# Kernel optimization log

Measured on AMD Instinct MI355X. Metric: run time of the kernel, lower is better.

## Reference

```python
import jax, jax.numpy as jnp
import numpy as np

NUM_HEADS = 4
HID = 64
NUM_LAYERS = 3
NEG_SLOPE = 0.2  # PyG GATConv default


def setup_inputs() -> dict:
    key = jax.random.key(0)
    ks = jax.random.split(key, 6)
    B, N, D = 64, 512, 64
    return {
        "embeddings": jax.random.normal(ks[0], (B, N, D), jnp.float32),
        "lin_w": jax.random.normal(ks[1], (NUM_LAYERS, NUM_HEADS * HID, D), jnp.float32) * 0.1,
        "att_src": jax.random.normal(ks[2], (NUM_LAYERS, NUM_HEADS, HID), jnp.float32) * 0.1,
        "att_dst": jax.random.normal(ks[3], (NUM_LAYERS, NUM_HEADS, HID), jnp.float32) * 0.1,
        "conv_b": jnp.zeros((NUM_LAYERS, HID), jnp.float32),
        "readout_w": jax.random.normal(ks[4], (D, HID), jnp.float32) * 0.1,
        "readout_b": jnp.zeros((D,), jnp.float32),
    }


def reference(embeddings, lin_w, att_src, att_dst, conv_b, readout_w, readout_b):
    # Graph is fully connected (combinations + reversed) and PyG GATConv adds
    # self-loops by default -> attention softmax over ALL nodes j for each i.
    B, N, _ = embeddings.shape
    x = embeddings
    for l in range(NUM_LAYERS):
        h = jnp.einsum('bnd,od->bno', x, lin_w[l]).reshape(B, N, NUM_HEADS, HID)  # [B,N,H,C]
        a_src = jnp.einsum('bnhc,hc->bnh', h, att_src[l])  # per source node j
        a_dst = jnp.einsum('bnhc,hc->bnh', h, att_dst[l])  # per target node i
        e = a_dst[:, :, None, :] + a_src[:, None, :, :]    # [B,i,j,H]
        e = jnp.where(e >= 0, e, NEG_SLOPE * e)            # LeakyReLU(0.2)
        alpha = jax.nn.softmax(e, axis=2)                  # softmax over neighbors j
        out = jnp.einsum('bijh,bjhc->bihc', alpha, h).mean(axis=2) + conv_b[l]  # concat=False -> head mean
        x = jax.nn.relu(out)
    pooled = x.mean(axis=1)                                # mean over nodes
    return pooled @ readout_w.T + readout_b                # [B, D]
```

## Files before the change

### kernel.cpp

```cpp
#include <hip/hip_runtime.h>
#include <math.h>


using short8  = __attribute__((ext_vector_type(8))) short;
using floatx4 = __attribute__((ext_vector_type(4))) float;

__device__ inline unsigned short f2bf(float f) {
    union { float f; unsigned u; } v; v.f = f;
    unsigned u = v.u + 0x7FFFu + ((v.u >> 16) & 1u);
    return (unsigned short)(u >> 16);
}
__device__ inline float bf2f(unsigned short s) {
    union { float f; unsigned u; } v; v.u = ((unsigned)s) << 16;
    return v.f;
}

__device__ inline void cvt8(const float4 a, const float4 b, short8& hi, short8& lo) {
    float f[8] = {a.x, a.y, a.z, a.w, b.x, b.y, b.z, b.w};
    short8 H, L;
#pragma unroll
    for (int i = 0; i < 8; ++i) {
        unsigned short h = f2bf(f[i]);
        H[i] = (short)h;
        L[i] = (short)f2bf(f[i] - bf2f(h));
    }
    hi = H; lo = L;
}

__global__ __launch_bounds__(256) void linprep_kernel(const float* __restrict__ x,
                                                      const float* __restrict__ W,
                                                      const float* __restrict__ att_src,
                                                      const float* __restrict__ att_dst,
                                                      float* __restrict__ hT,
                                                      int* __restrict__ g_rank,
                                                      float* __restrict__ g_E1,
                                                      float* __restrict__ g_E2,
                                                      float* __restrict__ g_aZ,
                                                      float* __restrict__ g_bZ,
                                                      int* __restrict__ g_k) {
    __shared__ unsigned short WH[64 * 72], WL[64 * 72];
    __shared__ float sA[512], dA[512];
    __shared__ int   s_idxE[512];
    __shared__ float z1suf[513], z2pre[513];
    __shared__ float wred[8];

    const int t  = threadIdx.x;
    const int bh = blockIdx.x;
    const int b  = bh >> 2;
    const int ct = bh & 3;
    const int c0 = ct * 64;

#pragma unroll
    for (int q = 0; q < 4; ++q) {
        int f = q * 256 + t;
        int wrow = f >> 4, d4 = f & 15;
        float4 v = *(const float4*)(W + (size_t)(c0 + wrow) * 64 + d4 * 4);
        unsigned short h0 = f2bf(v.x), h1 = f2bf(v.y), h2 = f2bf(v.z), h3 = f2bf(v.w);
        ushort4 hi = make_ushort4(h0, h1, h2, h3);
        ushort4 lo = make_ushort4(f2bf(v.x - bf2f(h0)), f2bf(v.y - bf2f(h1)),
                                  f2bf(v.z - bf2f(h2)), f2bf(v.w - bf2f(h3)));
        *(ushort4*)&WH[wrow * 72 + d4 * 4] = hi;
        *(ushort4*)&WL[wrow * 72 + d4 * 4] = lo;
    }
    __syncthreads();

    const int lane = t & 63, wv = t >> 6;
    const int mrow = lane & 15, quad = lane >> 4;

    short8 bhf[4][2], blf[4][2];
#pragma unroll
    for (int g = 0; g < 4; ++g)
#pragma unroll
        for (int kk = 0; kk < 2; ++kk) {
            int ko = kk * 32 + quad * 8;
            bhf[g][kk] = *(const short8*)&WH[(g * 16 + mrow) * 72 + ko];
            blf[g][kk] = *(const short8*)&WL[(g * 16 + mrow) * 72 + ko];
        }
    float as_g[4], ad_g[4];
#pragma unroll
    for (int g = 0; g < 4; ++g) {
        as_g[g] = att_src[c0 + g * 16 + mrow];
        ad_g[g] = att_dst[c0 + g * 16 + mrow];
    }

    const float* xbase = x + (size_t)(b * 512 + mrow) * 64 + quad * 8;
    float4 nxa = *(const float4*)(xbase + (size_t)wv * 1024);
    float4 nxb = *(const float4*)(xbase + (size_t)wv * 1024 + 4);
    float4 nxc = *(const float4*)(xbase + (size_t)wv * 1024 + 32);
    float4 nxd = *(const float4*)(xbase + (size_t)wv * 1024 + 36);

#pragma unroll 1
    for (int tl = wv; tl < 32; tl += 4) {
        float4 xa = nxa, xb = nxb, xc = nxc, xd = nxd;
        if (tl + 4 < 32) {
            const float* nb = xbase + (size_t)(tl + 4) * 1024;
            nxa = *(const float4*)(nb);
            nxb = *(const float4*)(nb + 4);
            nxc = *(const float4*)(nb + 32);
            nxd = *(const float4*)(nb + 36);
        }
        short8 ah0, al0, ah1, al1;
        cvt8(xa, xb, ah0, al0);
        cvt8(xc, xd, ah1, al1);

        floatx4 acc[4];
#pragma unroll
        for (int g = 0; g < 4; ++g) {
            floatx4 a = {0.f, 0.f, 0.f, 0.f};
            a = __builtin_amdgcn_mfma_f32_16x16x32_bf16(ah0, bhf[g][0], a, 0, 0, 0);
            a = __builtin_amdgcn_mfma_f32_16x16x32_bf16(ah1, bhf[g][1], a, 0, 0, 0);
            a = __builtin_amdgcn_mfma_f32_16x16x32_bf16(ah0, blf[g][0], a, 0, 0, 0);
            a = __builtin_amdgcn_mfma_f32_16x16x32_bf16(ah1, blf[g][1], a, 0, 0, 0);
            a = __builtin_amdgcn_mfma_f32_16x16x32_bf16(al0, bhf[g][0], a, 0, 0, 0);
            a = __builtin_amdgcn_mfma_f32_16x16x32_bf16(al1, bhf[g][1], a, 0, 0, 0);
            acc[g] = a;
        }

        const int r0 = b * 512 + tl * 16;
#pragma unroll
        for (int g = 0; g < 4; ++g) {
            *(float4*)&hT[(size_t)(ct * 64 + g * 16 + mrow) * 32768 + r0 + quad * 4] =
                make_float4(acc[g][0], acc[g][1], acc[g][2], acc[g][3]);
        }

        float ps[4], pd[4];
#pragma unroll
        for (int reg = 0; reg < 4; ++reg) {
            ps[reg] = acc[0][reg] * as_g[0] + acc[1][reg] * as_g[1]
                    + acc[2][reg] * as_g[2] + acc[3][reg] * as_g[3];
            pd[reg] = acc[0][reg] * ad_g[0] + acc[1][reg] * ad_g[1]
                    + acc[2][reg] * ad_g[2] + acc[3][reg] * ad_g[3];
        }
#pragma unroll
        for (int m = 1; m <= 8; m <<= 1) {
#pragma unroll
            for (int reg = 0; reg < 4; ++reg) {
                ps[reg] += __shfl_xor(ps[reg], m, 64);
                pd[reg] += __shfl_xor(pd[reg], m, 64);
            }
        }
        if (mrow < 4) {
            sA[tl * 16 + quad * 4 + mrow] = ps[mrow];
            dA[tl * 16 + quad * 4 + mrow] = pd[mrow];
        }
    }
    __syncthreads();

    const int wid = t >> 6;

    float dreg[2];
    for (int rr = 0; rr < 2; ++rr) dreg[rr] = dA[t + rr * 256];

    float v0 = sA[2 * t], v1 = sA[2 * t + 1];
    int id0 = 2 * t, id1 = 2 * t + 1;
    for (int k = 2; k <= 512; k <<= 1) {
        for (int j = k >> 1; j >= 1; j >>= 1) {
            bool asc = ((t & (k >> 1)) == 0);
            if (j == 1) {
                bool sw = asc ? (v0 > v1) : (v0 < v1);
                if (sw) { float tv = v0; v0 = v1; v1 = tv; int ti = id0; id0 = id1; id1 = ti; }
            } else if (j <= 64) {
                int m = j >> 1;
                float w0 = __shfl_xor(v0, m, 64);
                int  wi0 = __shfl_xor(id0, m, 64);
                float w1 = __shfl_xor(v1, m, 64);
                int  wi1 = __shfl_xor(id1, m, 64);
                bool low = ((t & m) == 0);
                bool wantmin = (low == asc);
                if (wantmin ? (w0 < v0) : (w0 > v0)) { v0 = w0; id0 = wi0; }
                if (wantmin ? (w1 < v1) : (w1 > v1)) { v1 = w1; id1 = wi1; }
            } else {
                int m = j >> 1;
                sA[2 * t] = v0; sA[2 * t + 1] = v1;
                s_idxE[2 * t] = id0; s_idxE[2 * t + 1] = id1;
                __syncthreads();
                int tp = t ^ m;
                float w0 = sA[2 * tp], w1 = sA[2 * tp + 1];
                int wi0 = s_idxE[2 * tp], wi1 = s_idxE[2 * tp + 1];
                bool low = ((t & m) == 0);
                bool wantmin = (low == asc);
                if (wantmin ? (w0 < v0) : (w0 > v0)) { v0 = w0; id0 = wi0; }
                if (wantmin ? (w1 < v1) : (w1 > v1)) { v1 = w1; id1 = wi1; }
                __syncthreads();
            }
        }
    }

    sA[2 * t] = v0; sA[2 * t + 1] = v1;
    __syncthreads();
    const float M = sA[511];
    float e1_0 = __expf(v0 - M), e1_1 = __expf(v1 - M);
    float e2_0 = __expf(0.2f * (v0 - M)), e2_1 = __expf(0.2f * (v1 - M));
    {
        const int base = bh * 512;
        g_E1[base + id0] = e1_0;  g_E1[base + id1] = e1_1;
        g_E2[base + id0] = e2_0;  g_E2[base + id1] = e2_1;
        g_rank[base + id0] = 2 * t;  g_rank[base + id1] = 2 * t + 1;
    }

    float S1 = e1_0 + e1_1, S2 = e2_0 + e2_1;
    float i1 = S1, i2 = S2;
    for (int off = 1; off < 64; off <<= 1) {
        float u1 = __shfl_up(i1, off, 64);
        float u2 = __shfl_up(i2, off, 64);
        if (lane >= off) { i1 += u1; i2 += u2; }
    }
    if (lane == 63) { wred[wid] = i1; wred[4 + wid] = i2; }
    __syncthreads();
    float off1 = 0.f, off2 = 0.f;
    for (int w = 0; w < wid; ++w) { off1 += wred[w]; off2 += wred[4 + w]; }
    const float T1 = wred[0] + wred[1] + wred[2] + wred[3];
    const float T2 = wred[4] + wred[5] + wred[6] + wred[7];
    float pre1 = off1 + i1 - S1;
    float pre2 = off2 + i2 - S2;
    z1suf[2 * t] = T1 - pre1;
    z1suf[2 * t + 1] = T1 - pre1 - e1_0;
    z2pre[2 * t] = pre2;
    z2pre[2 * t + 1] = pre2 + e2_0;
    if (t == 0) { z1suf[512] = 0.f; z2pre[512] = T2; }
    __syncthreads();

    for (int rr = 0; rr < 2; ++rr) {
        int i = t + rr * 256;
        float d = dreg[rr];
        int lo = 0, hi = 512;
        while (lo < hi) {
            int mid = (lo + hi) >> 1;
            if (d + sA[mid] >= 0.f) hi = mid; else lo = mid + 1;
        }
        int k = lo;
        float g = d + M;
        float G = (g >= 0.f) ? g : 0.2f * g;
        float al = __expf(g - G);
        float be = __expf(0.2f * g - G);
        float Z = al * z1suf[k] + be * z2pre[k];
        float inv = 1.0f / Z;
        g_aZ[bh * 512 + i] = al * inv;
        g_bZ[bh * 512 + i] = be * inv;
        g_k[bh * 512 + i]  = k;
    }
}

__global__ __launch_bounds__(256) void attn_agg_fin(const float* __restrict__ hT,
                                                    const int* __restrict__ g_rank,
                                                    const float* __restrict__ g_E1,
                                                    const float* __restrict__ g_E2,
                                                    const float* __restrict__ g_aZ,
                                                    const float* __restrict__ g_bZ,
                                                    const int* __restrict__ g_k,
                                                    const float* __restrict__ bias,
                                                    float* __restrict__ x) {
    const int b  = blockIdx.x & 63;
    const int cg = blockIdx.x >> 6;
    const int c0 = cg * 2;
    const int t = threadIdx.x;
    const int lane = t & 63, wv = t >> 6;

    __shared__ float A1[4][2][512], A2[4][2][512];
    __shared__ float tots[4][2];

    {
        const int bh = b * 4 + wv;
        const int base = bh * 512;
        const float* hTb = hT + (size_t)(wv * 64 + c0) * 32768 + (size_t)b * 512;
#pragma unroll
        for (int it = 0; it < 8; ++it) {
            int j = it * 64 + lane;
            int rk = g_rank[base + j];
            float e1 = g_E1[base + j];
            float e2 = g_E2[base + j];
            float h0 = hTb[j];
            float h1 = hTb[32768 + j];
            int pk = ((rk & 7) << 6) | (rk >> 3);
            A1[wv][0][pk] = e1 * h0;  A2[wv][0][pk] = e2 * h0;
            A1[wv][1][pk] = e1 * h1;  A2[wv][1][pk] = e2 * h1;
        }
#pragma unroll
        for (int cc = 0; cc < 2; ++cc) {
            float v1[8], v2[8];
#pragma unroll
            for (int i = 0; i < 8; ++i) {
                v1[i] = A1[wv][cc][i * 64 + lane];
                v2[i] = A2[wv][cc][i * 64 + lane];
            }
            float s1 = 0.f, s2 = 0.f;
#pragma unroll
            for (int i = 0; i < 8; ++i) { s1 += v1[i]; s2 += v2[i]; }
            float suf = s1;
#pragma unroll
            for (int off = 1; off < 64; off <<= 1) {
                float u = __shfl_down(suf, off, 64);
                if (lane + off < 64) suf += u;
            }
            float run = suf - s1;
            float pre = s2;
#pragma unroll
            for (int off = 1; off < 64; off <<= 1) {
                float u = __shfl_up(pre, off, 64);
                if (lane >= off) pre += u;
            }
            float run2 = pre - s2;
            if (lane == 63) tots[wv][cc] = pre;
#pragma unroll
            for (int i = 7; i >= 0; --i) { run += v1[i]; v1[i] = run; }
#pragma unroll
            for (int i = 0; i < 8; ++i) { float tv = v2[i]; v2[i] = run2; run2 += tv; }
#pragma unroll
            for (int i = 0; i < 8; ++i) {
                A1[wv][cc][i * 64 + lane] = v1[i];
                A2[wv][cc][i * 64 + lane] = v2[i];
            }
        }
    }
    __syncthreads();

    const float bv0 = bias[c0], bv1 = bias[c0 + 1];
#pragma unroll
    for (int rr = 0; rr < 2; ++rr) {
        const int i = t + rr * 256;
        float a0 = 0.f, a1 = 0.f;
#pragma unroll
        for (int head = 0; head < 4; ++head) {
            const int base = (b * 4 + head) * 512;
            float aZ = g_aZ[base + i];
            float bZ = g_bZ[base + i];
            int k = g_k[base + i];
            if (k < 512) {
                int pk = ((k & 7) << 6) | (k >> 3);
                a0 += aZ * A1[head][0][pk] + bZ * A2[head][0][pk];
                a1 += aZ * A1[head][1][pk] + bZ * A2[head][1][pk];
            } else {
                a0 += bZ * tots[head][0];
                a1 += bZ * tots[head][1];
            }
        }
        float2 o = make_float2(fmaxf(0.25f * a0 + bv0, 0.f),
                               fmaxf(0.25f * a1 + bv1, 0.f));
        *(float2*)&x[(size_t)(b * 512 + i) * 64 + c0] = o;
    }
}

__global__ __launch_bounds__(256) void readout_kernel(const float* __restrict__ x,
                                                      const float* __restrict__ rw,
                                                      const float* __restrict__ rb,
                                                      float* __restrict__ out) {
    __shared__ float red[4][64];
    __shared__ float pooled[64];
    int b = blockIdx.x, t = threadIdx.x;
    int c = t & 63, q = t >> 6;
    float acc = 0.f;
    for (int n = q; n < 512; n += 4) acc += x[((size_t)b * 512 + n) * 64 + c];
    red[q][c] = acc;
    __syncthreads();
    if (t < 64) pooled[t] = (red[0][t] + red[1][t] + red[2][t] + red[3][t]) * (1.0f / 512.0f);
    __syncthreads();
    if (t < 64) {
        float a = rb[t];
        for (int cc = 0; cc < 64; ++cc) a += pooled[cc] * rw[t * 64 + cc];
        out[b * 64 + t] = a;
    }
}

extern "C" void kernel_launch(void* const* d_in, const int* in_sizes, int n_in,
                              void* d_out, int out_size, void* d_ws, size_t ws_size,
                              hipStream_t stream) {
    const float* emb       = (const float*)d_in[0];
    const float* lin_w     = (const float*)d_in[1];
    const float* att_src   = (const float*)d_in[2];
    const float* att_dst   = (const float*)d_in[3];
    const float* conv_b    = (const float*)d_in[4];
    const float* readout_w = (const float*)d_in[5];
    const float* readout_b = (const float*)d_in[6];
    float* out = (float*)d_out;

    float* ws   = (float*)d_ws;
    float* xbuf = ws;
    float* hT   = ws + 2097152;
    float* meta = ws + 10485760;

    int*   g_rank = (int*)meta;
    float* g_E1   = meta + 131072;
    float* g_E2   = meta + 262144;
    float* g_aZ   = meta + 393216;
    float* g_bZ   = meta + 524288;
    int*   g_k    = (int*)(meta + 655360);

    for (int l = 0; l < 3; ++l) {
        const float* xin = (l == 0) ? emb : xbuf;
        linprep_kernel<<<256, 256, 0, stream>>>(xin, lin_w + (size_t)l * 16384,
                                                att_src + l * 256, att_dst + l * 256,
                                                hT, g_rank, g_E1, g_E2, g_aZ, g_bZ, g_k);
        attn_agg_fin<<<2048, 256, 0, stream>>>(hT, g_rank, g_E1, g_E2, g_aZ, g_bZ, g_k,
                                               conv_b + l * 64, xbuf);
    }
    readout_kernel<<<64, 256, 0, stream>>>(xbuf, readout_w, readout_b, out);
}
```

Measured before the change: 237.2 us.

## Fuse linear, attention prep and aggregation into one per-batch layer kernel

Merges the linear/prep kernel and the aggregation kernel into a single kernel with one 1024-thread block per batch element, each 256-thread group handling one head. The sort results, exponentials, normalizers and rank indices now stay in LDS instead of round-tripping through global memory, and one launch per layer is removed. In exchange the grid shrinks from hundreds or thousands of blocks to 64, leaving most CUs idle. Aggregation over the 64 channels now runs as 16 serial chunks with block-wide barriers.

```diff
diff --git a/kernel.cpp b/kernel.cpp
--- a/kernel.cpp
+++ b/kernel.cpp
@@ -27,34 +27,39 @@
     hi = H; lo = L;
 }
 
-__global__ __launch_bounds__(256) void linprep_kernel(const float* __restrict__ x,
-                                                      const float* __restrict__ W,
-                                                      const float* __restrict__ att_src,
-                                                      const float* __restrict__ att_dst,
-                                                      float* __restrict__ hT,
-                                                      int* __restrict__ g_rank,
-                                                      float* __restrict__ g_E1,
-                                                      float* __restrict__ g_E2,
-                                                      float* __restrict__ g_aZ,
-                                                      float* __restrict__ g_bZ,
-                                                      int* __restrict__ g_k) {
-    __shared__ unsigned short WH[64 * 72], WL[64 * 72];
-    __shared__ float sA[512], dA[512];
-    __shared__ int   s_idxE[512];
-    __shared__ float z1suf[513], z2pre[513];
-    __shared__ float wred[8];
-
-    const int t  = threadIdx.x;
-    const int bh = blockIdx.x;
-    const int b  = bh >> 2;
-    const int ct = bh & 3;
-    const int c0 = ct * 64;
+__global__ __launch_bounds__(1024, 4) void layer_kernel(
+        const float* __restrict__ x,
+        const float* __restrict__ W,
+        const float* __restrict__ att_src,
+        const float* __restrict__ att_dst,
+        const float* __restrict__ bias,
+        float* __restrict__ hT,
+        float* __restrict__ xout) {
+    __shared__ __align__(16) unsigned char uni[73728];
+    __shared__ float sA[4][512], dA[4][512];
+    __shared__ float E1s[4][512], E2s[4][512];
+    __shared__ int   rnks[4][512];
+    __shared__ float aZs[4][512], bZs[4][512];
+    __shared__ int   kks[4][512];
+    __shared__ float tots[4][4];
+    __shared__ float wred[4][8];
+
+    const int t     = threadIdx.x;
+    const int b     = blockIdx.x;
+    const int tg    = t >> 8;
+    const int tl256 = t & 255;
+    const int lane  = t & 63;
+    const int wq    = (t >> 6) & 3;
+    const int c0    = tg * 64;
+
+    unsigned short* WH = (unsigned short*)uni;
+    unsigned short* WL = WH + 256 * 72;
 
 #pragma unroll
     for (int q = 0; q < 4; ++q) {
-        int f = q * 256 + t;
+        int f = q * 1024 + t;
         int wrow = f >> 4, d4 = f & 15;
-        float4 v = *(const float4*)(W + (size_t)(c0 + wrow) * 64 + d4 * 4);
+        float4 v = *(const float4*)(W + (size_t)wrow * 64 + d4 * 4);
         unsigned short h0 = f2bf(v.x), h1 = f2bf(v.y), h2 = f2bf(v.z), h3 = f2bf(v.w);
         ushort4 hi = make_ushort4(h0, h1, h2, h3);
         ushort4 lo = make_ushort4(f2bf(v.x - bf2f(h0)), f2bf(v.y - bf2f(h1)),
@@ -64,18 +69,7 @@
     }
     __syncthreads();
 
-    const int lane = t & 63, wv = t >> 6;
     const int mrow = lane & 15, quad = lane >> 4;
-
-    short8 bhf[4][2], blf[4][2];
-#pragma unroll
-    for (int g = 0; g < 4; ++g)
-#pragma unroll
-        for (int kk = 0; kk < 2; ++kk) {
-            int ko = kk * 32 + quad * 8;
-            bhf[g][kk] = *(const short8*)&WH[(g * 16 + mrow) * 72 + ko];
-            blf[g][kk] = *(const short8*)&WL[(g * 16 + mrow) * 72 + ko];
-        }
     float as_g[4], ad_g[4];
 #pragma unroll
     for (int g = 0; g < 4; ++g) {
@@ -83,14 +77,15 @@
         ad_g[g] = att_dst[c0 + g * 16 + mrow];
     }
 
+    float* hTb = hT + (size_t)b * 131072;
     const float* xbase = x + (size_t)(b * 512 + mrow) * 64 + quad * 8;
-    float4 nxa = *(const float4*)(xbase + (size_t)wv * 1024);
-    float4 nxb = *(const float4*)(xbase + (size_t)wv * 1024 + 4);
-    float4 nxc = *(const float4*)(xbase + (size_t)wv * 1024 + 32);
-    float4 nxd = *(const float4*)(xbase + (size_t)wv * 1024 + 36);
+    float4 nxa = *(const float4*)(xbase + (size_t)wq * 1024);
+    float4 nxb = *(const float4*)(xbase + (size_t)wq * 1024 + 4);
+    float4 nxc = *(const float4*)(xbase + (size_t)wq * 1024 + 32);
+    float4 nxd = *(const float4*)(xbase + (size_t)wq * 1024 + 36);
 
 #pragma unroll 1
-    for (int tl = wv; tl < 32; tl += 4) {
+    for (int tl = wq; tl < 32; tl += 4) {
         float4 xa = nxa, xb = nxb, xc = nxc, xd = nxd;
         if (tl + 4 < 32) {
             const float* nb = xbase + (size_t)(tl + 4) * 1024;
@@ -106,20 +101,24 @@
         floatx4 acc[4];
 #pragma unroll
         for (int g = 0; g < 4; ++g) {
+            const int wr = (c0 + g * 16 + mrow) * 72;
+            short8 bh0 = *(const short8*)&WH[wr + quad * 8];
+            short8 bh1 = *(const short8*)&WH[wr + 32 + quad * 8];
+            short8 bl0 = *(const short8*)&WL[wr + quad * 8];
+            short8 bl1 = *(const short8*)&WL[wr + 32 + quad * 8];
             floatx4 a = {0.f, 0.f, 0.f, 0.f};
-            a = __builtin_amdgcn_mfma_f32_16x16x32_bf16(ah0, bhf[g][0], a, 0, 0, 0);
-            a = __builtin_amdgcn_mfma_f32_16x16x32_bf16(ah1, bhf[g][1], a, 0, 0, 0);
-            a = __builtin_amdgcn_mfma_f32_16x16x32_bf16(ah0, blf[g][0], a, 0, 0, 0);
-            a = __builtin_amdgcn_mfma_f32_16x16x32_bf16(ah1, blf[g][1], a, 0, 0, 0);
-            a = __builtin_amdgcn_mfma_f32_16x16x32_bf16(al0, bhf[g][0], a, 0, 0, 0);
-            a = __builtin_amdgcn_mfma_f32_16x16x32_bf16(al1, bhf[g][1], a, 0, 0, 0);
+            a = __builtin_amdgcn_mfma_f32_16x16x32_bf16(ah0, bh0, a, 0, 0, 0);
+            a = __builtin_amdgcn_mfma_f32_16x16x32_bf16(ah1, bh1, a, 0, 0, 0);
+            a = __builtin_amdgcn_mfma_f32_16x16x32_bf16(ah0, bl0, a, 0, 0, 0);
+            a = __builtin_amdgcn_mfma_f32_16x16x32_bf16(ah1, bl1, a, 0, 0, 0);
+            a = __builtin_amdgcn_mfma_f32_16x16x32_bf16(al0, bh0, a, 0, 0, 0);
+            a = __builtin_amdgcn_mfma_f32_16x16x32_bf16(al1, bh1, a, 0, 0, 0);
             acc[g] = a;
         }
 
-        const int r0 = b * 512 + tl * 16;
 #pragma unroll
         for (int g = 0; g < 4; ++g) {
-            *(float4*)&hT[(size_t)(ct * 64 + g * 16 + mrow) * 32768 + r0 + quad * 4] =
+            *(float4*)&hTb[(size_t)(c0 + g * 16 + mrow) * 512 + tl * 16 + quad * 4] =
                 make_float4(acc[g][0], acc[g][1], acc[g][2], acc[g][3]);
         }
 
@@ -140,22 +139,25 @@
             }
         }
         if (mrow < 4) {
-            sA[tl * 16 + quad * 4 + mrow] = ps[mrow];
-            dA[tl * 16 + quad * 4 + mrow] = pd[mrow];
-        }
-    }
-    __syncthreads();
-
-    const int wid = t >> 6;
+            sA[tg][tl * 16 + quad * 4 + mrow] = ps[mrow];
+            dA[tg][tl * 16 + quad * 4 + mrow] = pd[mrow];
+        }
+    }
+    __syncthreads();
+
+    int*   sidx = (int*)uni;
+    float* z1   = (float*)(uni + 8192);
+    float* z2   = (float*)(uni + 8192 + 8208);
+    const int wid = wq;
 
     float dreg[2];
-    for (int rr = 0; rr < 2; ++rr) dreg[rr] = dA[t + rr * 256];
-
-    float v0 = sA[2 * t], v1 = sA[2 * t + 1];
-    int id0 = 2 * t, id1 = 2 * t + 1;
+    for (int rr = 0; rr < 2; ++rr) dreg[rr] = dA[tg][tl256 + rr * 256];
+
+    float v0 = sA[tg][2 * tl256], v1 = sA[tg][2 * tl256 + 1];
+    int id0 = 2 * tl256, id1 = 2 * tl256 + 1;
     for (int k = 2; k <= 512; k <<= 1) {
         for (int j = k >> 1; j >= 1; j >>= 1) {
-            bool asc = ((t & (k >> 1)) == 0);
+            bool asc = ((tl256 & (k >> 1)) == 0);
             if (j == 1) {
                 bool sw = asc ? (v0 > v1) : (v0 < v1);
                 if (sw) { float tv = v0; v0 = v1; v1 = tv; int ti = id0; id0 = id1; id1 = ti; }
@@ -165,19 +167,19 @@
                 int  wi0 = __shfl_xor(id0, m, 64);
                 float w1 = __shfl_xor(v1, m, 64);
                 int  wi1 = __shfl_xor(id1, m, 64);
-                bool low = ((t & m) == 0);
+                bool low = ((tl256 & m) == 0);
                 bool wantmin = (low == asc);
                 if (wantmin ? (w0 < v0) : (w0 > v0)) { v0 = w0; id0 = wi0; }
                 if (wantmin ? (w1 < v1) : (w1 > v1)) { v1 = w1; id1 = wi1; }
             } else {
                 int m = j >> 1;
-                sA[2 * t] = v0; sA[2 * t + 1] = v1;
-                s_idxE[2 * t] = id0; s_idxE[2 * t + 1] = id1;
+                sA[tg][2 * tl256] = v0; sA[tg][2 * tl256 + 1] = v1;
+                sidx[tg * 512 + 2 * tl256] = id0; sidx[tg * 512 + 2 * tl256 + 1] = id1;
                 __syncthreads();
-                int tp = t ^ m;
-                float w0 = sA[2 * tp], w1 = sA[2 * tp + 1];
-                int wi0 = s_idxE[2 * tp], wi1 = s_idxE[2 * tp + 1];
-                bool low = ((t & m) == 0);
+                int tp = tl256 ^ m;
+                float w0 = sA[tg][2 * tp], w1 = sA[tg][2 * tp + 1];
+                int wi0 = sidx[tg * 512 + 2 * tp], wi1 = sidx[tg * 512 + 2 * tp + 1];
+                bool low = ((tl256 & m) == 0);
                 bool wantmin = (low == asc);
                 if (wantmin ? (w0 < v0) : (w0 > v0)) { v0 = w0; id0 = wi0; }
                 if (wantmin ? (w1 < v1) : (w1 > v1)) { v1 = w1; id1 = wi1; }
@@ -186,16 +188,15 @@
         }
     }
 
-    sA[2 * t] = v0; sA[2 * t + 1] = v1;
-    __syncthreads();
-    const float M = sA[511];
+    sA[tg][2 * tl256] = v0; sA[tg][2 * tl256 + 1] = v1;
+    __syncthreads();
+    const float M = sA[tg][511];
     float e1_0 = __expf(v0 - M), e1_1 = __expf(v1 - M);
     float e2_0 = __expf(0.2f * (v0 - M)), e2_1 = __expf(0.2f * (v1 - M));
     {
-        const int base = bh * 512;
-        g_E1[base + id0] = e1_0;  g_E1[base + id1] = e1_1;
-        g_E2[base + id0] = e2_0;  g_E2[base + id1] = e2_1;
-        g_rank[base + id0] = 2 * t;  g_rank[base + id1] = 2 * t + 1;
+        E1s[tg][id0] = e1_0;  E1s[tg][id1] = e1_1;
+        E2s[tg][id0] = e2_0;  E2s[tg][id1] = e2_1;
+        rnks[tg][id0] = 2 * tl256;  rnks[tg][id1] = 2 * tl256 + 1;
     }
 
     float S1 = e1_0 + e1_1, S2 = e2_0 + e2_1;
@@ -205,87 +206,73 @@
         float u2 = __shfl_up(i2, off, 64);
         if (lane >= off) { i1 += u1; i2 += u2; }
     }
-    if (lane == 63) { wred[wid] = i1; wred[4 + wid] = i2; }
+    if (lane == 63) { wred[tg][wid] = i1; wred[tg][4 + wid] = i2; }
     __syncthreads();
     float off1 = 0.f, off2 = 0.f;
-    for (int w = 0; w < wid; ++w) { off1 += wred[w]; off2 += wred[4 + w]; }
-    const float T1 = wred[0] + wred[1] + wred[2] + wred[3];
-    const float T2 = wred[4] + wred[5] + wred[6] + wred[7];
+    for (int w = 0; w < wid; ++w) { off1 += wred[tg][w]; off2 += wred[tg][4 + w]; }
+    const float T1 = wred[tg][0] + wred[tg][1] + wred[tg][2] + wred[tg][3];
+    const float T2 = wred[tg][4] + wred[tg][5] + wred[tg][6] + wred[tg][7];
     float pre1 = off1 + i1 - S1;
     float pre2 = off2 + i2 - S2;
-    z1suf[2 * t] = T1 - pre1;
-    z1suf[2 * t + 1] = T1 - pre1 - e1_0;
-    z2pre[2 * t] = pre2;
-    z2pre[2 * t + 1] = pre2 + e2_0;
-    if (t == 0) { z1suf[512] = 0.f; z2pre[512] = T2; }
+    z1[tg * 513 + 2 * tl256] = T1 - pre1;
+    z1[tg * 513 + 2 * tl256 + 1] = T1 - pre1 - e1_0;
+    z2[tg * 513 + 2 * tl256] = pre2;
+    z2[tg * 513 + 2 * tl256 + 1] = pre2 + e2_0;
+    if (tl256 == 0) { z1[tg * 513 + 512] = 0.f; z2[tg * 513 + 512] = T2; }
     __syncthreads();
 
     for (int rr = 0; rr < 2; ++rr) {
-        int i = t + rr * 256;
+        int i = tl256 + rr * 256;
         float d = dreg[rr];
         int lo = 0, hi = 512;
         while (lo < hi) {
             int mid = (lo + hi) >> 1;
-            if (d + sA[mid] >= 0.f) hi = mid; else lo = mid + 1;
+            if (d + sA[tg][mid] >= 0.f) hi = mid; else lo = mid + 1;
         }
         int k = lo;
         float g = d + M;
         float G = (g >= 0.f) ? g : 0.2f * g;
         float al = __expf(g - G);
         float be = __expf(0.2f * g - G);
-        float Z = al * z1suf[k] + be * z2pre[k];
+        float Z = al * z1[tg * 513 + k] + be * z2[tg * 513 + k];
         float inv = 1.0f / Z;
-        g_aZ[bh * 512 + i] = al * inv;
-        g_bZ[bh * 512 + i] = be * inv;
-        g_k[bh * 512 + i]  = k;
-    }
-}
-
-__global__ __launch_bounds__(256) void attn_agg_fin(const float* __restrict__ hT,
-                                                    const int* __restrict__ g_rank,
-                                                    const float* __restrict__ g_E1,
-                                                    const float* __restrict__ g_E2,
-                                                    const float* __restrict__ g_aZ,
-                                                    const float* __restrict__ g_bZ,
-                                                    const int* __restrict__ g_k,
-                                                    const float* __restrict__ bias,
-                                                    float* __restrict__ x) {
-    const int b  = blockIdx.x & 63;
-    const int cg = blockIdx.x >> 6;
-    const int c0 = cg * 2;
-    const int t = threadIdx.x;
-    const int lane = t & 63, wv = t >> 6;
-
-    __shared__ float A1[4][2][512], A2[4][2][512];
-    __shared__ float tots[4][2];
-
-    {
-        const int bh = b * 4 + wv;
-        const int base = bh * 512;
-        const float* hTb = hT + (size_t)(wv * 64 + c0) * 32768 + (size_t)b * 512;
-#pragma unroll
-        for (int it = 0; it < 8; ++it) {
-            int j = it * 64 + lane;
-            int rk = g_rank[base + j];
-            float e1 = g_E1[base + j];
-            float e2 = g_E2[base + j];
-            float h0 = hTb[j];
-            float h1 = hTb[32768 + j];
-            int pk = ((rk & 7) << 6) | (rk >> 3);
-            A1[wv][0][pk] = e1 * h0;  A2[wv][0][pk] = e2 * h0;
-            A1[wv][1][pk] = e1 * h1;  A2[wv][1][pk] = e2 * h1;
-        }
-#pragma unroll
-        for (int cc = 0; cc < 2; ++cc) {
-            float v1[8], v2[8];
+        aZs[tg][i] = al * inv;
+        bZs[tg][i] = be * inv;
+        kks[tg][i] = k;
+    }
+    __syncthreads();
+
+    float* A1 = (float*)uni;
+    float* A2 = (float*)(uni + 32768);
+    const int chp = t & 3, iq = t >> 2;
+
+#pragma unroll 1
+    for (int chunk = 0; chunk < 16; ++chunk) {
+        {
+            const int ch = chunk * 4 + wq;
+            float* T1p = A1 + (tg * 4 + wq) * 512;
+            float* T2p = A2 + (tg * 4 + wq) * 512;
+            const float* hTc = hTb + (size_t)(c0 + ch) * 512;
+#pragma unroll
+            for (int it = 0; it < 8; ++it) {
+                int j = it * 64 + lane;
+                int rk = rnks[tg][j];
+                float e1 = E1s[tg][j];
+                float e2 = E2s[tg][j];
+                float hv = hTc[j];
+                int pk = ((rk & 7) << 6) | (rk >> 3);
+                T1p[pk] = e1 * hv;
+                T2p[pk] = e2 * hv;
+            }
+            float v1s[8], v2s[8];
 #pragma unroll
             for (int i = 0; i < 8; ++i) {
-                v1[i] = A1[wv][cc][i * 64 + lane];
-                v2[i] = A2[wv][cc][i * 64 + lane];
+                v1s[i] = T1p[i * 64 + lane];
+                v2s[i] = T2p[i * 64 + lane];
             }
             float s1 = 0.f, s2 = 0.f;
 #pragma unroll
-            for (int i = 0; i < 8; ++i) { s1 += v1[i]; s2 += v2[i]; }
+            for (int i = 0; i < 8; ++i) { s1 += v1s[i]; s2 += v2s[i]; }
             float suf = s1;
 #pragma unroll
             for (int off = 1; off < 64; off <<= 1) {
@@ -300,43 +287,43 @@
                 if (lane >= off) pre += u;
             }
             float run2 = pre - s2;
-            if (lane == 63) tots[wv][cc] = pre;
-#pragma unroll
-            for (int i = 7; i >= 0; --i) { run += v1[i]; v1[i] = run; }
-#pragma unroll
-            for (int i = 0; i < 8; ++i) { float tv = v2[i]; v2[i] = run2; run2 += tv; }
+            if (lane == 63) tots[tg][wq] = pre;
+#pragma unroll
+            for (int i = 7; i >= 0; --i) { run += v1s[i]; v1s[i] = run; }
+#pragma unroll
+            for (int i = 0; i < 8; ++i) { float tv = v2s[i]; v2s[i] = run2; run2 += tv; }
 #pragma unroll
             for (int i = 0; i < 8; ++i) {
-                A1[wv][cc][i * 64 + lane] = v1[i];
-                A2[wv][cc][i * 64 + lane] = v2[i];
-            }
-        }
-    }
-    __syncthreads();
-
-    const float bv0 = bias[c0], bv1 = bias[c0 + 1];
-#pragma unroll
-    for (int rr = 0; rr < 2; ++rr) {
-        const int i = t + rr * 256;
-        float a0 = 0.f, a1 = 0.f;
-#pragma unroll
-        for (int head = 0; head < 4; ++head) {
-            const int base = (b * 4 + head) * 512;
-            float aZ = g_aZ[base + i];
-            float bZ = g_bZ[base + i];
-            int k = g_k[base + i];
-            if (k < 512) {
-                int pk = ((k & 7) << 6) | (k >> 3);
-                a0 += aZ * A1[head][0][pk] + bZ * A2[head][0][pk];
-                a1 += aZ * A1[head][1][pk] + bZ * A2[head][1][pk];
-            } else {
-                a0 += bZ * tots[head][0];
-                a1 += bZ * tots[head][1];
-            }
-        }
-        float2 o = make_float2(fmaxf(0.25f * a0 + bv0, 0.f),
-                               fmaxf(0.25f * a1 + bv1, 0.f));
-        *(float2*)&x[(size_t)(b * 512 + i) * 64 + c0] = o;
+                T1p[i * 64 + lane] = v1s[i];
+                T2p[i * 64 + lane] = v2s[i];
+            }
+        }
+        __syncthreads();
+
+        {
+            const int cq = chunk * 4 + chp;
+            const float bv = bias[cq];
+#pragma unroll
+            for (int rr = 0; rr < 2; ++rr) {
+                int i = iq + rr * 256;
+                float a = 0.f;
+#pragma unroll
+                for (int h = 0; h < 4; ++h) {
+                    float aZ = aZs[h][i];
+                    float bZ = bZs[h][i];
+                    int k = kks[h][i];
+                    if (k < 512) {
+                        int pk = ((k & 7) << 6) | (k >> 3);
+                        a += aZ * A1[(h * 4 + chp) * 512 + pk]
+                           + bZ * A2[(h * 4 + chp) * 512 + pk];
+                    } else {
+                        a += bZ * tots[h][chp];
+                    }
+                }
+                xout[(size_t)(b * 512 + i) * 64 + cq] = fmaxf(0.25f * a + bv, 0.f);
+            }
+        }
+        __syncthreads();
     }
 }
 
@@ -376,22 +363,12 @@
     float* ws   = (float*)d_ws;
     float* xbuf = ws;
     float* hT   = ws + 2097152;
-    float* meta = ws + 10485760;
-
-    int*   g_rank = (int*)meta;
-    float* g_E1   = meta + 131072;
-    float* g_E2   = meta + 262144;
-    float* g_aZ   = meta + 393216;
-    float* g_bZ   = meta + 524288;
-    int*   g_k    = (int*)(meta + 655360);
 
     for (int l = 0; l < 3; ++l) {
         const float* xin = (l == 0) ? emb : xbuf;
-        linprep_kernel<<<256, 256, 0, stream>>>(xin, lin_w + (size_t)l * 16384,
-                                                att_src + l * 256, att_dst + l * 256,
-                                                hT, g_rank, g_E1, g_E2, g_aZ, g_bZ, g_k);
-        attn_agg_fin<<<2048, 256, 0, stream>>>(hT, g_rank, g_E1, g_E2, g_aZ, g_bZ, g_k,
-                                               conv_b + l * 64, xbuf);
+        layer_kernel<<<64, 1024, 0, stream>>>(xin, lin_w + (size_t)l * 16384,
+                                              att_src + l * 256, att_dst + l * 256,
+                                              conv_b + l * 64, hT, xbuf);
     }
     readout_kernel<<<64, 256, 0, stream>>>(xbuf, readout_w, readout_b, out);
 }
```

Result: slower. 532.4 us (+124.5%).
